# Optimization experiments

Measured on AMD Instinct MI355X. Metric: run time of the kernel, lower is better.

## Reference

```python
import math
import jax, jax.numpy as jnp
import numpy as np

B, QDIM, KDIM, EMBED, HEADS, H, W = 2, 192, 192, 256, 8, 48, 48


def setup_inputs() -> dict:
    key = jax.random.key(0)
    ks = jax.random.split(key, 8)
    s = 0.05
    return {
        "query": jax.random.normal(ks[0], (B, QDIM, H, W), dtype=jnp.float32),
        "key": jax.random.normal(ks[1], (B, KDIM, H, W), dtype=jnp.float32),
        "Wq": jax.random.normal(ks[2], (EMBED, QDIM), dtype=jnp.float32) * s,
        "bq": jax.random.normal(ks[3], (EMBED,), dtype=jnp.float32) * s,
        "Wk": jax.random.normal(ks[4], (EMBED, KDIM), dtype=jnp.float32) * s,
        "bk": jax.random.normal(ks[5], (EMBED,), dtype=jnp.float32) * s,
        "Wv": jax.random.normal(ks[6], (EMBED, KDIM), dtype=jnp.float32) * s,
        "bv": jax.random.normal(ks[7], (EMBED,), dtype=jnp.float32) * s,
        "num_heads": HEADS,
    }


def reference(query, key, Wq, bq, Wk, bk, Wv, bv, num_heads):
    b, qdim, h, w = query.shape
    L = h * w
    embed = Wq.shape[0]
    hd = embed // num_heads

    # (B, C, H, W) -> (B, L, C) raster order
    q = query.transpose(0, 2, 3, 1).reshape(b, L, qdim)
    k_in = key.transpose(0, 2, 3, 1).reshape(b, L, -1)

    q = q @ Wq.T + bq               # (B, L, E)
    v = k_in @ Wv.T + bv            # (B, L, E)
    k = k_in @ Wk.T + bk            # (B, L, E)

    q = q.reshape(b, L, num_heads, hd).transpose(0, 2, 1, 3)  # bhqd
    k = k.reshape(b, L, num_heads, hd).transpose(0, 2, 1, 3)  # bhkd
    v = v.reshape(b, L, num_heads, hd).transpose(0, 2, 1, 3)  # bhkd

    scores = jnp.einsum("bhqd,bhkd->bhqk", q, k) / math.sqrt(hd)
    # causal (square subsequent) mask: -inf strictly above diagonal
    idx = jnp.arange(L)
    neg = jnp.asarray(jnp.finfo(scores.dtype).min, scores.dtype)
    mask = jnp.where(idx[:, None] >= idx[None, :], jnp.zeros((), scores.dtype), neg)
    scores = scores + mask

    attn = jax.nn.softmax(scores, axis=-1)  # dropout p=0.0 (eval)
    x = jnp.einsum("bhqk,bhkd->bhqd", attn, v)  # (B, H, L, hd)

    # (B, H, L, hd) -> (B, H, hd, L) -> (B, E, h, w)
    out = x.transpose(0, 1, 3, 2).reshape(b, embed, h, w)
    return out
```

## Files before the change

kernel.cpp:

```cpp
#include <hip/hip_runtime.h>

#define LQ 2304
#define CIN 192
#define EMB 256
#define NH 8
#define HD 32

typedef __attribute__((ext_vector_type(8))) short short8;
typedef __attribute__((ext_vector_type(4))) short short4v;
typedef __attribute__((ext_vector_type(4))) float floatx4;
typedef __attribute__((ext_vector_type(16))) float f32x16;

__device__ __forceinline__ unsigned short f2bf(float f) {
  union { float f; unsigned u; } v; v.f = f;
  unsigned r = v.u + 0x7FFFu + ((v.u >> 16) & 1u);
  return (unsigned short)(r >> 16);
}
__device__ __forceinline__ unsigned cvtpk(float lo, float hi) {
  unsigned r;
  asm("v_cvt_pk_bf16_f32 %0, %1, %2" : "=v"(r) : "v"(lo), "v"(hi));
  return r;
}
__device__ __forceinline__ void plswap(unsigned& a, unsigned& b, int hi) {
#if __has_builtin(__builtin_amdgcn_permlane32_swap)
  auto r = __builtin_amdgcn_permlane32_swap((int)a, (int)b, false, false);
  a = (unsigned)r[0]; b = (unsigned)r[1];
#else
  unsigned pa = (unsigned)__shfl_xor((int)a, 32);
  unsigned pb = (unsigned)__shfl_xor((int)b, 32);
  unsigned na = hi ? pb : a;
  unsigned nb = hi ? b : pa;
  a = na; b = nb;
#endif
}
__device__ __forceinline__ float xmax(float x, int hi) {
  unsigned a = __float_as_uint(x), b = a;
  plswap(a, b, hi);
  return fmaxf(__uint_as_float(a), __uint_as_float(b));
}
__device__ __forceinline__ float xadd(float x, int hi) {
  unsigned a = __float_as_uint(x), b = a;
  plswap(a, b, hi);
  return __uint_as_float(a) + __uint_as_float(b);
}

__global__ __launch_bounds__(256) void k_qkv(
    const float* __restrict__ query, const float* __restrict__ key,
    const float* __restrict__ Wq, const float* __restrict__ Wk, const float* __restrict__ Wv,
    const float* __restrict__ bq, const float* __restrict__ bk, const float* __restrict__ bv,
    unsigned short* Qb, unsigned short* Kb, unsigned short* Vt) {
  __shared__ float tile[64][65];
  __shared__ unsigned short Xs[64][200];

  int proj = blockIdx.z % 3;
  int ehalf = blockIdx.z / 3;
  int b = blockIdx.y;
  int l0 = blockIdx.x * 64;
  const float* src  = (proj == 0) ? query : key;
  const float* Wf   = (proj == 0) ? Wq : (proj == 1 ? Wk : Wv);
  const float* bias = (proj == 0) ? bq : (proj == 1 ? bk : bv);
  const float alpha = (proj == 0) ? 0.25505653582177047f : 1.0f;

  int tid = threadIdx.x;
  const float* sp = src + (size_t)b * CIN * LQ;

  int j4 = (tid & 15) * 4, i0 = tid >> 4;
  int cc = tid & 63, li0 = tid >> 6;
  for (int ch = 0; ch < 3; ++ch) {
    int c0 = ch * 64;
    #pragma unroll
    for (int i = i0; i < 64; i += 16) {
      floatx4 v = *(const floatx4*)(sp + (size_t)(c0 + i) * LQ + l0 + j4);
      tile[i][j4] = v[0]; tile[i][j4 + 1] = v[1];
      tile[i][j4 + 2] = v[2]; tile[i][j4 + 3] = v[3];
    }
    __syncthreads();
    #pragma unroll
    for (int li = li0; li < 64; li += 4)
      Xs[li][c0 + cc] = f2bf(tile[cc][li]);
    __syncthreads();
  }

  int lane = tid & 63, w = tid >> 6;
  int g = lane >> 4, r16 = lane & 15;
  int e0 = ehalf * 128 + w * 32;

  floatx4 acc[2][4];
  #pragma unroll
  for (int a = 0; a < 2; ++a)
    #pragma unroll
    for (int ls = 0; ls < 4; ++ls) acc[a][ls] = (floatx4){0.f, 0.f, 0.f, 0.f};

  #pragma unroll
  for (int ks = 0; ks < CIN; ks += 32) {
    short8 wf[2];
    #pragma unroll
    for (int a = 0; a < 2; ++a) {
      const float* wp = Wf + (size_t)(e0 + a * 16 + r16) * CIN + ks + g * 8;
      floatx4 w0 = *(const floatx4*)(wp);
      floatx4 w1 = *(const floatx4*)(wp + 4);
      union { unsigned u[4]; short8 s; } pk;
      pk.u[0] = cvtpk(w0[0], w0[1]);
      pk.u[1] = cvtpk(w0[2], w0[3]);
      pk.u[2] = cvtpk(w1[0], w1[1]);
      pk.u[3] = cvtpk(w1[2], w1[3]);
      wf[a] = pk.s;
    }
    #pragma unroll
    for (int ls = 0; ls < 4; ++ls) {
      short8 xf = *(const short8*)&Xs[ls * 16 + r16][ks + g * 8];
      #pragma unroll
      for (int a = 0; a < 2; ++a)
        acc[a][ls] = __builtin_amdgcn_mfma_f32_16x16x32_bf16(wf[a], xf, acc[a][ls], 0, 0, 0);
    }
  }

  #pragma unroll
  for (int a = 0; a < 2; ++a) {
    int ebase = e0 + a * 16 + g * 4;
    int h = ebase >> 5, d0 = ebase & 31;
    #pragma unroll
    for (int ls = 0; ls < 4; ++ls) {
      int lg = l0 + ls * 16 + r16;
      if (proj < 2) {
        unsigned short* outp = (proj == 0) ? Qb : Kb;
        short4v pk;
        #pragma unroll
        for (int r = 0; r < 4; ++r)
          pk[r] = (short)f2bf((acc[a][ls][r] + bias[ebase + r]) * alpha);
        *(short4v*)(outp + ((size_t)(b * NH + h) * LQ + lg) * HD + d0) = pk;
      } else {
        #pragma unroll
        for (int r = 0; r < 4; ++r)
          Vt[((size_t)(b * NH + h) * HD + d0 + r) * LQ + lg] =
              f2bf(acc[a][ls][r] + bias[ebase + r]);
      }
    }
  }
}

__device__ __forceinline__ void softmax_pv(f32x16& c0, f32x16& c1, f32x16& O,
                                           float& m, float& sum,
                                           const short8* vf, int hi) {
  float mx;
  {
    float a0 = fmaxf(fmaxf(c0[0], c0[8]),  fmaxf(c1[0], c1[8]));
    float a1 = fmaxf(fmaxf(c0[1], c0[9]),  fmaxf(c1[1], c1[9]));
    float a2 = fmaxf(fmaxf(c0[2], c0[10]), fmaxf(c1[2], c1[10]));
    float a3 = fmaxf(fmaxf(c0[3], c0[11]), fmaxf(c1[3], c1[11]));
    float a4 = fmaxf(fmaxf(c0[4], c0[12]), fmaxf(c1[4], c1[12]));
    float a5 = fmaxf(fmaxf(c0[5], c0[13]), fmaxf(c1[5], c1[13]));
    float a6 = fmaxf(fmaxf(c0[6], c0[14]), fmaxf(c1[6], c1[14]));
    float a7 = fmaxf(fmaxf(c0[7], c0[15]), fmaxf(c1[7], c1[15]));
    mx = fmaxf(fmaxf(fmaxf(a0, a1), fmaxf(a2, a3)),
               fmaxf(fmaxf(a4, a5), fmaxf(a6, a7)));
  }
  mx = xmax(mx, hi);

  if (!__all(mx - m <= 8.0f)) {
    float mn = fmaxf(m, mx);
    float al = exp2f(m - mn);
    sum *= al;
    #pragma unroll
    for (int i = 0; i < 16; ++i) O[i] *= al;
    m = mn;
  }

  #pragma unroll
  for (int i = 0; i < 16; ++i) {
    c0[i] = exp2f(c0[i] - m);
    c1[i] = exp2f(c1[i] - m);
  }
  {
    float a0 = (c0[0] + c0[8])  + (c1[0] + c1[8]);
    float a1 = (c0[1] + c0[9])  + (c1[1] + c1[9]);
    float a2 = (c0[2] + c0[10]) + (c1[2] + c1[10]);
    float a3 = (c0[3] + c0[11]) + (c1[3] + c1[11]);
    float a4 = (c0[4] + c0[12]) + (c1[4] + c1[12]);
    float a5 = (c0[5] + c0[13]) + (c1[5] + c1[13]);
    float a6 = (c0[6] + c0[14]) + (c1[6] + c1[14]);
    float a7 = (c0[7] + c0[15]) + (c1[7] + c1[15]);
    float ts = ((a0 + a1) + (a2 + a3)) + ((a4 + a5) + (a6 + a7));
    sum += xadd(ts, hi);
  }

  union { unsigned u[4]; short8 s; } pA, pB, pC, pD;
  {
    unsigned a = cvtpk(c0[0], c0[1]), b = cvtpk(c0[2], c0[3]);
    unsigned c = cvtpk(c0[4], c0[5]), d = cvtpk(c0[6], c0[7]);
    plswap(a, c, hi); plswap(b, d, hi);
    pA.u[0] = a; pA.u[1] = b; pA.u[2] = c; pA.u[3] = d;
  }
  {
    unsigned a = cvtpk(c0[8], c0[9]),  b = cvtpk(c0[10], c0[11]);
    unsigned c = cvtpk(c0[12], c0[13]), d = cvtpk(c0[14], c0[15]);
    plswap(a, c, hi); plswap(b, d, hi);
    pB.u[0] = a; pB.u[1] = b; pB.u[2] = c; pB.u[3] = d;
  }
  {
    unsigned a = cvtpk(c1[0], c1[1]), b = cvtpk(c1[2], c1[3]);
    unsigned c = cvtpk(c1[4], c1[5]), d = cvtpk(c1[6], c1[7]);
    plswap(a, c, hi); plswap(b, d, hi);
    pC.u[0] = a; pC.u[1] = b; pC.u[2] = c; pC.u[3] = d;
  }
  {
    unsigned a = cvtpk(c1[8], c1[9]),  b = cvtpk(c1[10], c1[11]);
    unsigned c = cvtpk(c1[12], c1[13]), d = cvtpk(c1[14], c1[15]);
    plswap(a, c, hi); plswap(b, d, hi);
    pD.u[0] = a; pD.u[1] = b; pD.u[2] = c; pD.u[3] = d;
  }

  __builtin_amdgcn_s_setprio(1);
  O = __builtin_amdgcn_mfma_f32_32x32x16_bf16(vf[0], pA.s, O, 0, 0, 0);
  O = __builtin_amdgcn_mfma_f32_32x32x16_bf16(vf[1], pB.s, O, 0, 0, 0);
  O = __builtin_amdgcn_mfma_f32_32x32x16_bf16(vf[2], pC.s, O, 0, 0, 0);
  O = __builtin_amdgcn_mfma_f32_32x32x16_bf16(vf[3], pD.s, O, 0, 0, 0);
  __builtin_amdgcn_s_setprio(0);
}

__global__ __launch_bounds__(256, 4) void k_attn(const unsigned short* __restrict__ Qb,
                                                 const unsigned short* __restrict__ Kb,
                                                 const unsigned short* __restrict__ Vt,
                                                 float* __restrict__ out) {
  __shared__ float Osh[4][32][33];
  __shared__ float Msh[4][32];
  __shared__ float Ssh[4][32];

  int bid = blockIdx.x;
  int xcd = bid & 7;
  int idx = bid >> 3;
  int half = idx / 72;
  int j = 71 - (idx - half * 72);
  int bh = xcd + 8 * half;
  int q0b = j * 32;

  int w = threadIdx.x >> 6, lane = threadIdx.x & 63;
  int qcol = lane & 31, hi = lane >> 5;
  int qg = q0b + qcol;

  const unsigned short* Qrow = Qb + ((size_t)bh * LQ + qg) * HD + hi * 8;
  short8 qf0 = *(const short8*)(Qrow);
  short8 qf1 = *(const short8*)(Qrow + 16);

  const f32x16 Z16 = {0,0,0,0,0,0,0,0,0,0,0,0,0,0,0,0};
  f32x16 O = Z16;
  float m = -1e30f, sum = 0.f;

  const unsigned short* Kbase = Kb + (size_t)bh * LQ * HD;
  const unsigned short* Vbase = Vt + (size_t)bh * HD * LQ;
  int ntiles = (q0b + 95) >> 6;

  for (int t = w; t < ntiles; t += 4) {
    int k0 = t * 64;

    short8 kf[4], vf[4];
    {
      const unsigned short* kr = Kbase + (size_t)(k0 + qcol) * HD + hi * 8;
      kf[0] = *(const short8*)(kr);
      kf[1] = *(const short8*)(kr + 16);
      kf[2] = *(const short8*)(kr + 32 * HD);
      kf[3] = *(const short8*)(kr + 32 * HD + 16);
      const unsigned short* vr = Vbase + (size_t)qcol * LQ + k0 + hi * 8;
      vf[0] = *(const short8*)(vr);
      vf[1] = *(const short8*)(vr + 16);
      vf[2] = *(const short8*)(vr + 32);
      vf[3] = *(const short8*)(vr + 48);
    }

    __builtin_amdgcn_s_setprio(1);
    f32x16 c0 = __builtin_amdgcn_mfma_f32_32x32x16_bf16(kf[0], qf0, Z16, 0, 0, 0);
    c0 = __builtin_amdgcn_mfma_f32_32x32x16_bf16(kf[1], qf1, c0, 0, 0, 0);
    f32x16 c1 = __builtin_amdgcn_mfma_f32_32x32x16_bf16(kf[2], qf0, Z16, 0, 0, 0);
    c1 = __builtin_amdgcn_mfma_f32_32x32x16_bf16(kf[3], qf1, c1, 0, 0, 0);
    __builtin_amdgcn_s_setprio(0);

    if (t == ntiles - 1) {
      #pragma unroll
      for (int i = 0; i < 16; ++i) {
        int kg = k0 + (i & 3) + 8 * (i >> 2) + 4 * hi;
        if (kg > qg)      c0[i] = -1e30f;
        if (kg + 32 > qg) c1[i] = -1e30f;
      }
    }

    softmax_pv(c0, c1, O, m, sum, vf, hi);
  }

  #pragma unroll
  for (int i = 0; i < 16; ++i) {
    int d = (i & 3) + 8 * (i >> 2) + 4 * hi;
    Osh[w][d][qcol] = O[i];
  }
  if (hi == 0) { Msh[w][qcol] = m; Ssh[w][qcol] = sum; }
  __syncthreads();

  int tid = threadIdx.x;
  int q = tid & 31, dblk = tid >> 5;
  float m0 = Msh[0][q], m1 = Msh[1][q], m2 = Msh[2][q], m3 = Msh[3][q];
  float ms = fmaxf(fmaxf(m0, m1), fmaxf(m2, m3));
  float a0 = exp2f(m0 - ms), a1 = exp2f(m1 - ms);
  float a2 = exp2f(m2 - ms), a3 = exp2f(m3 - ms);
  float ss = a0 * Ssh[0][q] + a1 * Ssh[1][q] + a2 * Ssh[2][q] + a3 * Ssh[3][q];
  float inv = 1.0f / ss;
  #pragma unroll
  for (int r = 0; r < 4; ++r) {
    int d = dblk * 4 + r;
    float o = a0 * Osh[0][d][q] + a1 * Osh[1][d][q] +
              a2 * Osh[2][d][q] + a3 * Osh[3][d][q];
    out[((size_t)bh * HD + d) * LQ + q0b + q] = o * inv;
  }
}

extern "C" void kernel_launch(void* const* d_in, const int* in_sizes, int n_in,
                              void* d_out, int out_size, void* d_ws, size_t ws_size,
                              hipStream_t stream) {
  const float* query = (const float*)d_in[0];
  const float* key   = (const float*)d_in[1];
  const float* Wq    = (const float*)d_in[2];
  const float* bq    = (const float*)d_in[3];
  const float* Wk    = (const float*)d_in[4];
  const float* bk    = (const float*)d_in[5];
  const float* Wv    = (const float*)d_in[6];
  const float* bv    = (const float*)d_in[7];
  float* out = (float*)d_out;

  unsigned short* Qb = (unsigned short*)d_ws;
  unsigned short* Kb = Qb + 2 * NH * LQ * HD;
  unsigned short* Vt = Kb + 2 * NH * LQ * HD;

  hipLaunchKernelGGL(k_qkv, dim3(36, 2, 6), dim3(256), 0, stream,
                     query, key, Wq, Wk, Wv, bq, bk, bv, Qb, Kb, Vt);
  hipLaunchKernelGGL(k_attn, dim3(1152), dim3(256), 0, stream,
                     Qb, Kb, Vt, out);
}
```

Before: 41.37 us.

## Share K/V tiles across two query subtiles via double-buffered LDS staging

Each attention block now covers 64 queries, split as two 32-query subtiles times two key-parallel waves. K and V tiles are loaded cooperatively into swizzled, double-buffered shared memory and reused by both query subtiles, which roughly halves global K/V traffic, and the next tiles are prefetched while the current ones are computed. The grid is halved, the cross-wave merge is reduced to two partial results, and launch bounds drop to 3 blocks per CU. The cost is a block-wide barrier on every step and fewer blocks to balance the causal work.

Result: slower. 52.78 us (+27.6%).

```diff
diff --git a/kernel.cpp b/kernel.cpp
--- a/kernel.cpp
+++ b/kernel.cpp
@@ -218,25 +218,32 @@
   __builtin_amdgcn_s_setprio(0);
 }
 
-__global__ __launch_bounds__(256, 4) void k_attn(const unsigned short* __restrict__ Qb,
+__global__ __launch_bounds__(256, 3) void k_attn(const unsigned short* __restrict__ Qb,
                                                  const unsigned short* __restrict__ Kb,
                                                  const unsigned short* __restrict__ Vt,
                                                  float* __restrict__ out) {
-  __shared__ float Osh[4][32][33];
-  __shared__ float Msh[4][32];
-  __shared__ float Ssh[4][32];
+  __shared__ short8 Kls[2][2][256];
+  __shared__ short8 Vls[2][2][256];
+  __shared__ float Osh[2][32][33];
+  __shared__ float Msh[2][32];
+  __shared__ float Ssh[2][32];
 
   int bid = blockIdx.x;
   int xcd = bid & 7;
   int idx = bid >> 3;
-  int half = idx / 72;
-  int j = 71 - (idx - half * 72);
+  int half = idx / 36;
+  int j = 35 - (idx - half * 36);
   int bh = xcd + 8 * half;
-  int q0b = j * 32;
-
-  int w = threadIdx.x >> 6, lane = threadIdx.x & 63;
+  int q0b = j * 64;
+  int ntiles = j + 1;
+  int steps = (ntiles + 1) >> 1;
+
+  int tid = threadIdx.x;
+  int w = tid >> 6, lane = tid & 63;
+  int qs = w & 1, p = w >> 1;
   int qcol = lane & 31, hi = lane >> 5;
-  int qg = q0b + qcol;
+  int qg = q0b + qs * 32 + qcol;
+  int qmin = q0b + qs * 32;
 
   const unsigned short* Qrow = Qb + ((size_t)bh * LQ + qg) * HD + hi * 8;
   short8 qf0 = *(const short8*)(Qrow);
@@ -248,66 +255,110 @@
 
   const unsigned short* Kbase = Kb + (size_t)bh * LQ * HD;
   const unsigned short* Vbase = Vt + (size_t)bh * HD * LQ;
-  int ntiles = (q0b + 95) >> 6;
-
-  for (int t = w; t < ntiles; t += 4) {
-    int k0 = t * 64;
-
-    short8 kf[4], vf[4];
-    {
-      const unsigned short* kr = Kbase + (size_t)(k0 + qcol) * HD + hi * 8;
-      kf[0] = *(const short8*)(kr);
-      kf[1] = *(const short8*)(kr + 16);
-      kf[2] = *(const short8*)(kr + 32 * HD);
-      kf[3] = *(const short8*)(kr + 32 * HD + 16);
-      const unsigned short* vr = Vbase + (size_t)qcol * LQ + k0 + hi * 8;
-      vf[0] = *(const short8*)(vr);
-      vf[1] = *(const short8*)(vr + 16);
-      vf[2] = *(const short8*)(vr + 32);
-      vf[3] = *(const short8*)(vr + 48);
-    }
-
-    __builtin_amdgcn_s_setprio(1);
-    f32x16 c0 = __builtin_amdgcn_mfma_f32_32x32x16_bf16(kf[0], qf0, Z16, 0, 0, 0);
-    c0 = __builtin_amdgcn_mfma_f32_32x32x16_bf16(kf[1], qf1, c0, 0, 0, 0);
-    f32x16 c1 = __builtin_amdgcn_mfma_f32_32x32x16_bf16(kf[2], qf0, Z16, 0, 0, 0);
-    c1 = __builtin_amdgcn_mfma_f32_32x32x16_bf16(kf[3], qf1, c1, 0, 0, 0);
-    __builtin_amdgcn_s_setprio(0);
-
-    if (t == ntiles - 1) {
+
+  int kx = (qcol >> 1) & 3;
+  int koff[4], voff[4];
+  #pragma unroll
+  for (int f = 0; f < 4; ++f)
+    koff[f] = (qcol + 32 * (f >> 1)) * 4 + (((f & 1) * 2 + hi) ^ kx);
+  #pragma unroll
+  for (int i = 0; i < 4; ++i)
+    voff[i] = qcol * 8 + ((i * 2 + hi) ^ (qcol & 7));
+
+  int sr = tid >> 2, su = tid & 3;
+  int vr = tid >> 3, vu = tid & 7;
+  int kunit = sr * 4 + (su ^ ((sr >> 1) & 3));
+  int vunit = vr * 8 + (vu ^ (vr & 7));
+
+  {
+    short8 a = *(const short8*)(Kbase + (size_t)sr * HD + su * 8);
+    short8 b = *(const short8*)(Vbase + (size_t)vr * LQ + vu * 8);
+    Kls[0][0][kunit] = a;
+    Vls[0][0][vunit] = b;
+    if (1 < ntiles) {
+      short8 c = *(const short8*)(Kbase + (size_t)(64 + sr) * HD + su * 8);
+      short8 d = *(const short8*)(Vbase + (size_t)vr * LQ + 64 + vu * 8);
+      Kls[0][1][kunit] = c;
+      Vls[0][1][vunit] = d;
+    }
+  }
+  __syncthreads();
+
+  for (int s = 0; s < steps; ++s) {
+    int b = s & 1;
+    bool pf = (s + 1 < steps);
+    int nt0 = 2 * (s + 1);
+    bool pf1 = pf && (nt0 + 1 < ntiles);
+
+    short8 nK0, nV0, nK1, nV1;
+    if (pf) {
+      nK0 = *(const short8*)(Kbase + (size_t)(nt0 * 64 + sr) * HD + su * 8);
+      nV0 = *(const short8*)(Vbase + (size_t)vr * LQ + nt0 * 64 + vu * 8);
+    }
+    if (pf1) {
+      nK1 = *(const short8*)(Kbase + (size_t)((nt0 + 1) * 64 + sr) * HD + su * 8);
+      nV1 = *(const short8*)(Vbase + (size_t)vr * LQ + (nt0 + 1) * 64 + vu * 8);
+    }
+
+    int t = 2 * s + p;
+    if (t < ntiles) {
+      int k0 = t * 64;
+      short8 kf[4], vf[4];
       #pragma unroll
-      for (int i = 0; i < 16; ++i) {
-        int kg = k0 + (i & 3) + 8 * (i >> 2) + 4 * hi;
-        if (kg > qg)      c0[i] = -1e30f;
-        if (kg + 32 > qg) c1[i] = -1e30f;
+      for (int f = 0; f < 4; ++f) kf[f] = Kls[b][p][koff[f]];
+      #pragma unroll
+      for (int i = 0; i < 4; ++i) vf[i] = Vls[b][p][voff[i]];
+
+      __builtin_amdgcn_s_setprio(1);
+      f32x16 c0 = __builtin_amdgcn_mfma_f32_32x32x16_bf16(kf[0], qf0, Z16, 0, 0, 0);
+      c0 = __builtin_amdgcn_mfma_f32_32x32x16_bf16(kf[1], qf1, c0, 0, 0, 0);
+      f32x16 c1 = __builtin_amdgcn_mfma_f32_32x32x16_bf16(kf[2], qf0, Z16, 0, 0, 0);
+      c1 = __builtin_amdgcn_mfma_f32_32x32x16_bf16(kf[3], qf1, c1, 0, 0, 0);
+      __builtin_amdgcn_s_setprio(0);
+
+      if (k0 + 63 > qmin) {
+        #pragma unroll
+        for (int i = 0; i < 16; ++i) {
+          int kg = k0 + (i & 3) + 8 * (i >> 2) + 4 * hi;
+          if (kg > qg)      c0[i] = -1e30f;
+          if (kg + 32 > qg) c1[i] = -1e30f;
+        }
       }
-    }
-
-    softmax_pv(c0, c1, O, m, sum, vf, hi);
-  }
-
-  #pragma unroll
-  for (int i = 0; i < 16; ++i) {
-    int d = (i & 3) + 8 * (i >> 2) + 4 * hi;
-    Osh[w][d][qcol] = O[i];
-  }
-  if (hi == 0) { Msh[w][qcol] = m; Ssh[w][qcol] = sum; }
+      softmax_pv(c0, c1, O, m, sum, vf, hi);
+    }
+
+    if (pf) {
+      Kls[b ^ 1][0][kunit] = nK0;
+      Vls[b ^ 1][0][vunit] = nV0;
+    }
+    if (pf1) {
+      Kls[b ^ 1][1][kunit] = nK1;
+      Vls[b ^ 1][1][vunit] = nV1;
+    }
+    __syncthreads();
+  }
+
+  if (p == 1) {
+    #pragma unroll
+    for (int i = 0; i < 16; ++i) {
+      int d = (i & 3) + 8 * (i >> 2) + 4 * hi;
+      Osh[qs][d][qcol] = O[i];
+    }
+    if (hi == 0) { Msh[qs][qcol] = m; Ssh[qs][qcol] = sum; }
+  }
   __syncthreads();
-
-  int tid = threadIdx.x;
-  int q = tid & 31, dblk = tid >> 5;
-  float m0 = Msh[0][q], m1 = Msh[1][q], m2 = Msh[2][q], m3 = Msh[3][q];
-  float ms = fmaxf(fmaxf(m0, m1), fmaxf(m2, m3));
-  float a0 = exp2f(m0 - ms), a1 = exp2f(m1 - ms);
-  float a2 = exp2f(m2 - ms), a3 = exp2f(m3 - ms);
-  float ss = a0 * Ssh[0][q] + a1 * Ssh[1][q] + a2 * Ssh[2][q] + a3 * Ssh[3][q];
-  float inv = 1.0f / ss;
-  #pragma unroll
-  for (int r = 0; r < 4; ++r) {
-    int d = dblk * 4 + r;
-    float o = a0 * Osh[0][d][q] + a1 * Osh[1][d][q] +
-              a2 * Osh[2][d][q] + a3 * Osh[3][d][q];
-    out[((size_t)bh * HD + d) * LQ + q0b + q] = o * inv;
+  if (p == 0) {
+    float m1 = Msh[qs][qcol], s1 = Ssh[qs][qcol];
+    float ms = fmaxf(m, m1);
+    float a0 = exp2f(m - ms), a1 = exp2f(m1 - ms);
+    float ss = a0 * sum + a1 * s1;
+    float inv = 1.0f / ss;
+    #pragma unroll
+    for (int i = 0; i < 16; ++i) {
+      int d = (i & 3) + 8 * (i >> 2) + 4 * hi;
+      float o = a0 * O[i] + a1 * Osh[qs][d][qcol];
+      out[((size_t)bh * HD + d) * LQ + qg] = o * inv;
+    }
   }
 }
 
@@ -330,6 +381,6 @@
 
   hipLaunchKernelGGL(k_qkv, dim3(36, 2, 6), dim3(256), 0, stream,
                      query, key, Wq, Wk, Wv, bq, bk, bv, Qb, Kb, Vt);
-  hipLaunchKernelGGL(k_attn, dim3(1152), dim3(256), 0, stream,
+  hipLaunchKernelGGL(k_attn, dim3(576), dim3(256), 0, stream,
                      Qb, Kb, Vt, out);
 }
```

## Process 64 queries per attention block to reuse K/V tile loads

Applied to the files above, without the earlier changes.

Each attention block now handles two 32-query subtiles that share every loaded K and V tile, which halves the grid and halves global K/V traffic per query. The causal diagonal mask is applied per subtile, and the cross-wave merge through shared memory is widened to 64 queries. The cost is higher register pressure, with launch bounds lowered to three blocks per CU, and fewer blocks available to spread the triangular workload across CUs.

New measurement: 49.19 us. 18.9% more time.

```diff
diff --git a/kernel.cpp b/kernel.cpp
--- a/kernel.cpp
+++ b/kernel.cpp
@@ -218,37 +218,40 @@
   __builtin_amdgcn_s_setprio(0);
 }
 
-__global__ __launch_bounds__(256, 4) void k_attn(const unsigned short* __restrict__ Qb,
+__global__ __launch_bounds__(256, 3) void k_attn(const unsigned short* __restrict__ Qb,
                                                  const unsigned short* __restrict__ Kb,
                                                  const unsigned short* __restrict__ Vt,
                                                  float* __restrict__ out) {
-  __shared__ float Osh[4][32][33];
-  __shared__ float Msh[4][32];
-  __shared__ float Ssh[4][32];
+  __shared__ float Osh[4][32][65];
+  __shared__ float Msh[4][64];
+  __shared__ float Ssh[4][64];
 
   int bid = blockIdx.x;
   int xcd = bid & 7;
   int idx = bid >> 3;
-  int half = idx / 72;
-  int j = 71 - (idx - half * 72);
+  int half = idx / 36;
+  int j = 35 - (idx - half * 36);
   int bh = xcd + 8 * half;
-  int q0b = j * 32;
+  int q0b = j * 64;
+  int ntiles = j + 1;
 
   int w = threadIdx.x >> 6, lane = threadIdx.x & 63;
   int qcol = lane & 31, hi = lane >> 5;
-  int qg = q0b + qcol;
-
-  const unsigned short* Qrow = Qb + ((size_t)bh * LQ + qg) * HD + hi * 8;
-  short8 qf0 = *(const short8*)(Qrow);
-  short8 qf1 = *(const short8*)(Qrow + 16);
+  int qgA = q0b + qcol, qgB = q0b + 32 + qcol;
+
+  const unsigned short* QrowA = Qb + ((size_t)bh * LQ + qgA) * HD + hi * 8;
+  const unsigned short* QrowB = Qb + ((size_t)bh * LQ + qgB) * HD + hi * 8;
+  short8 qfA0 = *(const short8*)(QrowA);
+  short8 qfA1 = *(const short8*)(QrowA + 16);
+  short8 qfB0 = *(const short8*)(QrowB);
+  short8 qfB1 = *(const short8*)(QrowB + 16);
 
   const f32x16 Z16 = {0,0,0,0,0,0,0,0,0,0,0,0,0,0,0,0};
-  f32x16 O = Z16;
-  float m = -1e30f, sum = 0.f;
+  f32x16 OA = Z16, OB = Z16;
+  float mA = -1e30f, sA = 0.f, mB = -1e30f, sB = 0.f;
 
   const unsigned short* Kbase = Kb + (size_t)bh * LQ * HD;
   const unsigned short* Vbase = Vt + (size_t)bh * HD * LQ;
-  int ntiles = (q0b + 95) >> 6;
 
   for (int t = w; t < ntiles; t += 4) {
     int k0 = t * 64;
@@ -266,36 +269,57 @@
       vf[2] = *(const short8*)(vr + 32);
       vf[3] = *(const short8*)(vr + 48);
     }
-
-    __builtin_amdgcn_s_setprio(1);
-    f32x16 c0 = __builtin_amdgcn_mfma_f32_32x32x16_bf16(kf[0], qf0, Z16, 0, 0, 0);
-    c0 = __builtin_amdgcn_mfma_f32_32x32x16_bf16(kf[1], qf1, c0, 0, 0, 0);
-    f32x16 c1 = __builtin_amdgcn_mfma_f32_32x32x16_bf16(kf[2], qf0, Z16, 0, 0, 0);
-    c1 = __builtin_amdgcn_mfma_f32_32x32x16_bf16(kf[3], qf1, c1, 0, 0, 0);
-    __builtin_amdgcn_s_setprio(0);
-
-    if (t == ntiles - 1) {
-      #pragma unroll
-      for (int i = 0; i < 16; ++i) {
-        int kg = k0 + (i & 3) + 8 * (i >> 2) + 4 * hi;
-        if (kg > qg)      c0[i] = -1e30f;
-        if (kg + 32 > qg) c1[i] = -1e30f;
+    bool diag = (t == ntiles - 1);
+
+    {
+      __builtin_amdgcn_s_setprio(1);
+      f32x16 c0 = __builtin_amdgcn_mfma_f32_32x32x16_bf16(kf[0], qfA0, Z16, 0, 0, 0);
+      c0 = __builtin_amdgcn_mfma_f32_32x32x16_bf16(kf[1], qfA1, c0, 0, 0, 0);
+      f32x16 c1 = __builtin_amdgcn_mfma_f32_32x32x16_bf16(kf[2], qfA0, Z16, 0, 0, 0);
+      c1 = __builtin_amdgcn_mfma_f32_32x32x16_bf16(kf[3], qfA1, c1, 0, 0, 0);
+      __builtin_amdgcn_s_setprio(0);
+      if (diag) {
+        #pragma unroll
+        for (int i = 0; i < 16; ++i) {
+          int kg = k0 + (i & 3) + 8 * (i >> 2) + 4 * hi;
+          if (kg > qgA)      c0[i] = -1e30f;
+          if (kg + 32 > qgA) c1[i] = -1e30f;
+        }
       }
-    }
-
-    softmax_pv(c0, c1, O, m, sum, vf, hi);
+      softmax_pv(c0, c1, OA, mA, sA, vf, hi);
+    }
+    {
+      __builtin_amdgcn_s_setprio(1);
+      f32x16 c0 = __builtin_amdgcn_mfma_f32_32x32x16_bf16(kf[0], qfB0, Z16, 0, 0, 0);
+      c0 = __builtin_amdgcn_mfma_f32_32x32x16_bf16(kf[1], qfB1, c0, 0, 0, 0);
+      f32x16 c1 = __builtin_amdgcn_mfma_f32_32x32x16_bf16(kf[2], qfB0, Z16, 0, 0, 0);
+      c1 = __builtin_amdgcn_mfma_f32_32x32x16_bf16(kf[3], qfB1, c1, 0, 0, 0);
+      __builtin_amdgcn_s_setprio(0);
+      if (diag) {
+        #pragma unroll
+        for (int i = 0; i < 16; ++i) {
+          int kg = k0 + (i & 3) + 8 * (i >> 2) + 4 * hi;
+          if (kg > qgB)      c0[i] = -1e30f;
+          if (kg + 32 > qgB) c1[i] = -1e30f;
+        }
+      }
+      softmax_pv(c0, c1, OB, mB, sB, vf, hi);
+    }
   }
 
   #pragma unroll
   for (int i = 0; i < 16; ++i) {
     int d = (i & 3) + 8 * (i >> 2) + 4 * hi;
-    Osh[w][d][qcol] = O[i];
-  }
-  if (hi == 0) { Msh[w][qcol] = m; Ssh[w][qcol] = sum; }
+    Osh[w][d][qcol] = OA[i];
+    Osh[w][d][32 + qcol] = OB[i];
+  }
+  if (hi == 0) {
+    Msh[w][qcol] = mA; Ssh[w][qcol] = sA;
+    Msh[w][32 + qcol] = mB; Ssh[w][32 + qcol] = sB;
+  }
   __syncthreads();
 
-  int tid = threadIdx.x;
-  int q = tid & 31, dblk = tid >> 5;
+  int q = threadIdx.x & 63, dblk = threadIdx.x >> 6;
   float m0 = Msh[0][q], m1 = Msh[1][q], m2 = Msh[2][q], m3 = Msh[3][q];
   float ms = fmaxf(fmaxf(m0, m1), fmaxf(m2, m3));
   float a0 = exp2f(m0 - ms), a1 = exp2f(m1 - ms);
@@ -303,8 +327,8 @@
   float ss = a0 * Ssh[0][q] + a1 * Ssh[1][q] + a2 * Ssh[2][q] + a3 * Ssh[3][q];
   float inv = 1.0f / ss;
   #pragma unroll
-  for (int r = 0; r < 4; ++r) {
-    int d = dblk * 4 + r;
+  for (int r = 0; r < 8; ++r) {
+    int d = dblk * 8 + r;
     float o = a0 * Osh[0][d][q] + a1 * Osh[1][d][q] +
               a2 * Osh[2][d][q] + a3 * Osh[3][d][q];
     out[((size_t)bh * HD + d) * LQ + q0b + q] = o * inv;
@@ -330,6 +354,6 @@
 
   hipLaunchKernelGGL(k_qkv, dim3(36, 2, 6), dim3(256), 0, stream,
                      query, key, Wq, Wk, Wv, bq, bk, bv, Qb, Kb, Vt);
-  hipLaunchKernelGGL(k_attn, dim3(1152), dim3(256), 0, stream,
+  hipLaunchKernelGGL(k_attn, dim3(576), dim3(256), 0, stream,
                      Qb, Kb, Vt, out);
 }
```
